# Kernel optimization log

Hardware: AMD Instinct MI355X
Metric: run time of the kernel (lower is better)

## Reference

```python
import jax, jax.numpy as jnp
import numpy as np

D_MODEL = 1024
NHEAD = 16
HEAD_DIM = D_MODEL // NHEAD
LN_EPS = 1e-5


def _layer_norm(x, g, b):
    mu = jnp.mean(x, axis=-1, keepdims=True)
    var = jnp.var(x, axis=-1, keepdims=True)
    return (x - mu) * jax.lax.rsqrt(var + LN_EPS) * g + b


def setup_inputs() -> dict:
    key = jax.random.key(0)
    ks = jax.random.split(key, 12)
    B, S = 2, 2048
    init = 0.02
    return {
        "query": jax.random.normal(ks[0], (B, S, D_MODEL), jnp.float32),
        "key_": jax.random.normal(ks[1], (B, S, D_MODEL), jnp.float32),
        "value": jax.random.normal(ks[2], (B, S, D_MODEL), jnp.float32),
        "Wq": jax.random.normal(ks[3], (D_MODEL, D_MODEL), jnp.float32) * init,
        "bq": jnp.zeros((D_MODEL,), jnp.float32),
        "Wk": jax.random.normal(ks[4], (D_MODEL, D_MODEL), jnp.float32) * init,
        "bk": jnp.zeros((D_MODEL,), jnp.float32),
        "Wv": jax.random.normal(ks[5], (D_MODEL, D_MODEL), jnp.float32) * init,
        "bv": jnp.zeros((D_MODEL,), jnp.float32),
        "Wo": jax.random.normal(ks[6], (D_MODEL, D_MODEL), jnp.float32) * init,
        "bo": jnp.zeros((D_MODEL,), jnp.float32),
        "ln_g": jnp.ones((D_MODEL,), jnp.float32),
        "ln_b": jnp.zeros((D_MODEL,), jnp.float32),
    }


def reference(query, key_, value, Wq, bq, Wk, bk, Wv, bv, Wo, bo, ln_g, ln_b):
    B, T, D = query.shape
    S = key_.shape[1]
    # shared LayerNorm applied to q, k, v inputs (as in the torch module)
    qn = _layer_norm(query, ln_g, ln_b)
    kn = _layer_norm(key_, ln_g, ln_b)
    vn = _layer_norm(value, ln_g, ln_b)
    # projections (torch Linear: x @ W.T + b)
    q = qn @ Wq.T + bq
    k = kn @ Wk.T + bk
    v = vn @ Wv.T + bv
    # [B, H, S, Dh]
    q = q.reshape(B, T, NHEAD, HEAD_DIM).transpose(0, 2, 1, 3)
    k = k.reshape(B, S, NHEAD, HEAD_DIM).transpose(0, 2, 1, 3)
    v = v.reshape(B, S, NHEAD, HEAD_DIM).transpose(0, 2, 1, 3)
    q = q * (HEAD_DIM ** -0.5)
    # [B, H, T, S] score matrix (explicitly materialized, as in source)
    scores = jnp.einsum("bhtd,bhsd->bhts", q, k)
    causal = jnp.triu(jnp.ones((T, S), dtype=bool), k=1)
    scores = jnp.where(causal, -jnp.inf, scores)
    attn = jax.nn.softmax(scores.astype(jnp.float32), axis=-1).astype(query.dtype)
    out = jnp.einsum("bhts,bhsd->bhtd", attn, v)
    out = out.transpose(0, 2, 1, 3).reshape(B, T, D)
    out = out @ Wo.T + bo
    return out, attn
```

## Files before the change

### kernel.cpp

```cpp
#include <hip/hip_runtime.h>
#include <hip/hip_bf16.h>

typedef unsigned short u16;
typedef unsigned int u32;
typedef __bf16 bf16x8 __attribute__((ext_vector_type(8)));
typedef float f32x4 __attribute__((ext_vector_type(4)));

__device__ __forceinline__ u16 f2bf(float f) {
  __hip_bfloat16 h = __float2bfloat16(f);
  u16 u;
  __builtin_memcpy(&u, &h, 2);
  return u;
}

__device__ __forceinline__ void gload16(const u16* g, u16* l) {
  __builtin_amdgcn_global_load_lds(
      (const __attribute__((address_space(1))) u32*)g,
      (__attribute__((address_space(3))) u32*)l, 16, 0, 0);
}

__global__ __launch_bounds__(256) void ln_cast(
    const float* __restrict__ q, const float* __restrict__ k,
    const float* __restrict__ v, const float* __restrict__ g,
    const float* __restrict__ bb, u16* __restrict__ xn) {
  int row = blockIdx.x;
  int tsel = row >> 12;
  int r_in = row & 4095;
  const float* src = (tsel == 0) ? q : (tsel == 1) ? k : v;
  int tid = threadIdx.x;
  float4 x = ((const float4*)(src + (size_t)r_in * 1024))[tid];
  float s  = x.x + x.y + x.z + x.w;
  float ss = x.x * x.x + x.y * x.y + x.z * x.z + x.w * x.w;
  #pragma unroll
  for (int m = 1; m < 64; m <<= 1) { s += __shfl_xor(s, m); ss += __shfl_xor(ss, m); }
  __shared__ float red[8];
  int wid = tid >> 6;
  if ((tid & 63) == 0) { red[wid] = s; red[wid + 4] = ss; }
  __syncthreads();
  s  = red[0] + red[1] + red[2] + red[3];
  ss = red[4] + red[5] + red[6] + red[7];
  float mu  = s * (1.f / 1024.f);
  float var = ss * (1.f / 1024.f) - mu * mu;
  float rs  = rsqrtf(var + 1e-5f);
  float4 gv = ((const float4*)g)[tid];
  float4 bv = ((const float4*)bb)[tid];
  ushort4 o;
  o.x = f2bf((x.x - mu) * rs * gv.x + bv.x);
  o.y = f2bf((x.y - mu) * rs * gv.y + bv.y);
  o.z = f2bf((x.z - mu) * rs * gv.z + bv.z);
  o.w = f2bf((x.w - mu) * rs * gv.w + bv.w);
  ((ushort4*)(xn + (size_t)row * 1024))[tid] = o;
}

__global__ __launch_bounds__(256) void wcast(
    const float* __restrict__ wq, const float* __restrict__ wk,
    const float* __restrict__ wv, const float* __restrict__ wo,
    u16* __restrict__ dst) {
  int i = blockIdx.x * 256 + threadIdx.x;
  int e = i * 4;
  int sel = e >> 20;
  int loc = e & 1048575;
  const float* w = (sel == 0) ? wq : (sel == 1) ? wk : (sel == 2) ? wv : wo;
  float4 x = *(const float4*)(w + loc);
  ushort4 o;
  o.x = f2bf(x.x); o.y = f2bf(x.y); o.z = f2bf(x.z); o.w = f2bf(x.w);
  *(ushort4*)(dst + e) = o;
}

__global__ __launch_bounds__(256) void gemm_nt(
    const u16* __restrict__ A0, const u16* __restrict__ W0,
    const float* __restrict__ bias0, const float* __restrict__ bias1,
    const float* __restrict__ bias2,
    float* __restrict__ oF, u16* __restrict__ oP, u16* __restrict__ oVT,
    int mode) {
  __shared__ alignas(16) u16 Al[128][64];
  __shared__ alignas(16) u16 Bl[128][64];
  int z = blockIdx.z;
  const u16* A = A0 + (size_t)z * 4194304;
  const u16* W = W0 + (size_t)z * 1048576;
  const float* bias = (z == 0) ? bias0 : (z == 1) ? bias1 : bias2;
  int m0 = blockIdx.y * 128, n0 = blockIdx.x * 128;
  int tid = threadIdx.x;
  int lane = tid & 63, wid = tid >> 6;
  int wr = wid >> 1, wc = wid & 1;
  int l15 = lane & 15, lg = lane >> 4;
  int lr = lane >> 3, lc = lane & 7;

  f32x4 acc[4][4];
  #pragma unroll
  for (int i = 0; i < 4; ++i)
    #pragma unroll
    for (int j = 0; j < 4; ++j) acc[i][j] = (f32x4){0.f, 0.f, 0.f, 0.f};

  for (int kt = 0; kt < 1024; kt += 64) {
    __syncthreads();
    #pragma unroll
    for (int qq = 0; qq < 4; ++qq) {
      int rb = (qq * 4 + wid) * 8;
      gload16(A + (size_t)(m0 + rb + lr) * 1024 + kt + lc * 8, &Al[rb][0]);
      gload16(W + (size_t)(n0 + rb + lr) * 1024 + kt + lc * 8, &Bl[rb][0]);
    }
    __syncthreads();
    #pragma unroll
    for (int kb = 0; kb < 2; ++kb) {
      bf16x8 af[4], bw[4];
      #pragma unroll
      for (int i = 0; i < 4; ++i)
        af[i] = *(const bf16x8*)&Al[wr * 64 + i * 16 + l15][kb * 32 + lg * 8];
      #pragma unroll
      for (int j = 0; j < 4; ++j)
        bw[j] = *(const bf16x8*)&Bl[wc * 64 + j * 16 + l15][kb * 32 + lg * 8];
      #pragma unroll
      for (int i = 0; i < 4; ++i)
        #pragma unroll
        for (int j = 0; j < 4; ++j)
          acc[i][j] = __builtin_amdgcn_mfma_f32_16x16x32_bf16(af[i], bw[j], acc[i][j], 0, 0, 0);
    }
  }

  float scale = (mode == 1 && z == 0) ? 0.125f : 1.f;
  #pragma unroll
  for (int i = 0; i < 4; ++i) {
    #pragma unroll
    for (int j = 0; j < 4; ++j) {
      int n = n0 + wc * 64 + j * 16 + l15;
      float bn = bias[n];
      #pragma unroll
      for (int r = 0; r < 4; ++r) {
        int m = m0 + wr * 64 + i * 16 + lg * 4 + r;
        float val = (acc[i][j][r] + bn) * scale;
        if (mode == 0) {
          oF[(size_t)m * 1024 + n] = val;
        } else {
          int b = m >> 11, sIdx = m & 2047, h = n >> 6, d = n & 63;
          if (z == 2) {
            oVT[((size_t)((b * 16 + h) * 64 + d)) * 2048 + sIdx] = f2bf(val);
          } else {
            oP[(size_t)z * 4194304 +
               ((size_t)((b * 16 + h) * 2048 + sIdx)) * 64 + d] = f2bf(val);
          }
        }
      }
    }
  }
}

__global__ __launch_bounds__(256) void attn_kernel(
    const u16* __restrict__ proj, const u16* __restrict__ vt,
    float* __restrict__ attnOut, u16* __restrict__ oat,
    float* __restrict__ linvG) {
  __shared__ alignas(16) u16 Kl[64][64];
  __shared__ alignas(16) u16 Vt[64][64];
  __shared__ alignas(16) u16 Pl[4][16][72];
  const int t0 = blockIdx.x * 64;
  const int bh = blockIdx.y;
  const int tid = threadIdx.x;
  const int lane = tid & 63, w = tid >> 6;
  const int l15 = lane & 15, lg = lane >> 4;
  const int lr = lane >> 3, lc = lane & 7;
  const u16* Q = proj;
  const u16* K = proj + 4194304;
  const u16* VT = vt + (size_t)bh * 131072;

  float* attnB = attnOut + ((size_t)bh * 2048) * 2048;

  {
    const int zc0 = t0 + 64;
    const int rowLen = (2048 - zc0) >> 2;
    const float4 z4 = make_float4(0.f, 0.f, 0.f, 0.f);
    for (int r = w; r < 64; r += 4) {
      float4* rp = (float4*)(attnB + (size_t)(t0 + r) * 2048 + zc0);
      for (int cc = lane; cc < rowLen; cc += 64) rp[cc] = z4;
    }
  }

  bf16x8 qa[2];
  {
    size_t qoff = ((size_t)bh * 2048 + t0 + w * 16 + l15) * 64 + lg * 8;
    qa[0] = *(const bf16x8*)(Q + qoff);
    qa[1] = *(const bf16x8*)(Q + qoff + 32);
  }
  const int jmax = t0 >> 6;
  const int trow_qk = t0 + w * 16 + l15;

  float lsum = 0.f;
  f32x4 acc_o[4];
  #pragma unroll
  for (int c2 = 0; c2 < 4; ++c2) acc_o[c2] = (f32x4){0.f, 0.f, 0.f, 0.f};

  for (int j = 0; j <= jmax; ++j) {
    __syncthreads();
    #pragma unroll
    for (int qq = 0; qq < 2; ++qq) {
      int rb = (qq * 4 + w) * 8;
      gload16(K + ((size_t)bh * 2048 + j * 64 + rb + lr) * 64 + lc * 8, &Kl[rb][0]);
      gload16(VT + (size_t)(rb + lr) * 2048 + j * 64 + lc * 8, &Vt[rb][0]);
    }
    __syncthreads();
    #pragma unroll
    for (int c = 0; c < 4; ++c) {
      f32x4 s = {0.f, 0.f, 0.f, 0.f};
      #pragma unroll
      for (int kb = 0; kb < 2; ++kb) {
        bf16x8 ka = *(const bf16x8*)&Kl[c * 16 + l15][kb * 32 + lg * 8];
        s = __builtin_amdgcn_mfma_f32_16x16x32_bf16(ka, qa[kb], s, 0, 0, 0);
      }
      int col0 = j * 64 + c * 16 + lg * 4;
      float p[4];
      #pragma unroll
      for (int r = 0; r < 4; ++r) {
        float e = __expf(s[r]);
        p[r] = (col0 + r <= trow_qk) ? e : 0.f;
        lsum += p[r];
      }
      *(float4*)&attnB[(size_t)trow_qk * 2048 + col0] =
          make_float4(p[0], p[1], p[2], p[3]);
      ushort4 pk;
      pk.x = f2bf(p[0]); pk.y = f2bf(p[1]); pk.z = f2bf(p[2]); pk.w = f2bf(p[3]);
      *(ushort4*)&Pl[w][l15][c * 16 + lg * 4] = pk;
    }
    __syncthreads();
    #pragma unroll
    for (int kb = 0; kb < 2; ++kb) {
      bf16x8 pa = *(const bf16x8*)&Pl[w][l15][kb * 32 + lg * 8];
      #pragma unroll
      for (int c2 = 0; c2 < 4; ++c2) {
        bf16x8 bv = *(const bf16x8*)&Vt[c2 * 16 + l15][kb * 32 + lg * 8];
        acc_o[c2] = __builtin_amdgcn_mfma_f32_16x16x32_bf16(pa, bv, acc_o[c2], 0, 0, 0);
      }
    }
  }

  lsum += __shfl_xor(lsum, 16);
  lsum += __shfl_xor(lsum, 32);
  float linv = 1.f / lsum;
  if (lg == 0) linvG[(size_t)bh * 2048 + trow_qk] = linv;

  float linv_r[4];
  #pragma unroll
  for (int r = 0; r < 4; ++r) linv_r[r] = __shfl(linv, lg * 4 + r);

  int b = bh >> 4, h = bh & 15;
  #pragma unroll
  for (int c2 = 0; c2 < 4; ++c2) {
    #pragma unroll
    for (int r = 0; r < 4; ++r) {
      int trow = t0 + w * 16 + lg * 4 + r;
      oat[((size_t)(b * 2048 + trow)) * 1024 + h * 64 + c2 * 16 + l15] =
          f2bf(acc_o[c2][r] * linv_r[r]);
    }
  }
}

__global__ __launch_bounds__(256) void rescale_kernel(
    float* __restrict__ attnOut, const float* __restrict__ linvG) {
  const int t0 = blockIdx.x * 64;
  const int bh = blockIdx.y;
  const int tid = threadIdx.x;
  const int lane = tid & 63, w = tid >> 6;
  const int ncol4 = (t0 + 64) >> 2;
  float* attnB = attnOut + ((size_t)bh * 2048) * 2048;
  for (int r = w; r < 64; r += 4) {
    float li = linvG[(size_t)bh * 2048 + t0 + r];
    float4* rp = (float4*)(attnB + (size_t)(t0 + r) * 2048);
    for (int cc = lane; cc < ncol4; cc += 64) {
      float4 x = rp[cc];
      x.x *= li; x.y *= li; x.z *= li; x.w *= li;
      rp[cc] = x;
    }
  }
}

extern "C" void kernel_launch(void* const* d_in, const int* in_sizes, int n_in,
                              void* d_out, int out_size, void* d_ws, size_t ws_size,
                              hipStream_t stream) {
  const float* q    = (const float*)d_in[0];
  const float* k    = (const float*)d_in[1];
  const float* v    = (const float*)d_in[2];
  const float* Wq   = (const float*)d_in[3];
  const float* bq   = (const float*)d_in[4];
  const float* Wk   = (const float*)d_in[5];
  const float* bk   = (const float*)d_in[6];
  const float* Wv   = (const float*)d_in[7];
  const float* bv   = (const float*)d_in[8];
  const float* Wo   = (const float*)d_in[9];
  const float* bo   = (const float*)d_in[10];
  const float* ln_g = (const float*)d_in[11];
  const float* ln_b = (const float*)d_in[12];

  u16* ws   = (u16*)d_ws;
  u16* xn   = ws;
  u16* wb   = ws + 12582912;
  u16* proj = ws + 16777216;
  u16* vt   = ws + 25165824;
  u16* oat  = ws + 29360128;
  float* linvG = (float*)(ws + 33554432);
  float* out  = (float*)d_out;
  float* attn = out + 4194304;

  ln_cast<<<dim3(12288), dim3(256), 0, stream>>>(q, k, v, ln_g, ln_b, xn);
  wcast<<<dim3(4096), dim3(256), 0, stream>>>(Wq, Wk, Wv, Wo, wb);
  gemm_nt<<<dim3(8, 32, 3), dim3(256), 0, stream>>>(xn, wb, bq, bk, bv,
                                                    nullptr, proj, vt, 1);
  attn_kernel<<<dim3(32, 32), dim3(256), 0, stream>>>(proj, vt, attn, oat, linvG);
  rescale_kernel<<<dim3(32, 32), dim3(256), 0, stream>>>(attn, linvG);
  gemm_nt<<<dim3(8, 32, 1), dim3(256), 0, stream>>>(oat, wb + 3 * 1048576, bo,
                                                    bo, bo, out, nullptr, nullptr, 0);
}
```

Baseline: 918.1 us.

## Fuse attention-prob normalization into attention kernel via full-row LDS buffer

The attention kernel now keeps each block's unnormalized bf16 probability rows (32 query rows by 2048 keys) in shared memory. Once row sums are known, it writes the normalized fp32 attention matrix, zero tail included, in a single pass. This removes the separate rescale kernel and its read-modify-write of the large attention output. Blocks shrink to 32 query rows with 512 threads, and each wave handles one 16-column slice, with XOR swizzling of the LDS layouts. The risks are that the stored probabilities are now bf16-rounded before normalization, and that the roughly 128KB of LDS per block limits occupancy.

```diff
diff --git a/kernel.cpp b/kernel.cpp
--- a/kernel.cpp
+++ b/kernel.cpp
@@ -11,6 +11,12 @@
   u16 u;
   __builtin_memcpy(&u, &h, 2);
   return u;
+}
+__device__ __forceinline__ float bf2f(u16 u) {
+  u32 b = ((u32)u) << 16;
+  float f;
+  __builtin_memcpy(&f, &b, 4);
+  return f;
 }
 
 __device__ __forceinline__ void gload16(const u16* g, u16* l) {
@@ -145,128 +151,118 @@
   }
 }
 
-__global__ __launch_bounds__(256) void attn_kernel(
+__global__ __launch_bounds__(512) void attn_kernel(
     const u16* __restrict__ proj, const u16* __restrict__ vt,
-    float* __restrict__ attnOut, u16* __restrict__ oat,
-    float* __restrict__ linvG) {
+    float* __restrict__ attnOut, u16* __restrict__ oat) {
+  __shared__ alignas(16) u16 Ps[32][2048];
   __shared__ alignas(16) u16 Kl[64][64];
   __shared__ alignas(16) u16 Vt[64][64];
-  __shared__ alignas(16) u16 Pl[4][16][72];
-  const int t0 = blockIdx.x * 64;
-  const int bh = blockIdx.y;
+  __shared__ float lred[2][16][4];
+  __shared__ float linv_s[32];
+
+  const int bh = blockIdx.x;
+  const int tb = blockIdx.y;
+  const int t0 = tb * 32;
   const int tid = threadIdx.x;
-  const int lane = tid & 63, w = tid >> 6;
+  const int w = tid >> 6;
+  const int qt = w >> 2;
+  const int c  = w & 3;
+  const int lane = tid & 63;
   const int l15 = lane & 15, lg = lane >> 4;
   const int lr = lane >> 3, lc = lane & 7;
+  const int swz_src = ((lc ^ lr) * 8);
+
   const u16* Q = proj;
   const u16* K = proj + 4194304;
-  const u16* VT = vt + (size_t)bh * 131072;
-
-  float* attnB = attnOut + ((size_t)bh * 2048) * 2048;
-
-  {
-    const int zc0 = t0 + 64;
-    const int rowLen = (2048 - zc0) >> 2;
-    const float4 z4 = make_float4(0.f, 0.f, 0.f, 0.f);
-    for (int r = w; r < 64; r += 4) {
-      float4* rp = (float4*)(attnB + (size_t)(t0 + r) * 2048 + zc0);
-      for (int cc = lane; cc < rowLen; cc += 64) rp[cc] = z4;
-    }
-  }
+  const u16* VTg = vt + (size_t)bh * 131072;
 
   bf16x8 qa[2];
   {
-    size_t qoff = ((size_t)bh * 2048 + t0 + w * 16 + l15) * 64 + lg * 8;
+    size_t qoff = ((size_t)bh * 2048 + t0 + qt * 16 + l15) * 64 + lg * 8;
     qa[0] = *(const bf16x8*)(Q + qoff);
     qa[1] = *(const bf16x8*)(Q + qoff + 32);
   }
-  const int jmax = t0 >> 6;
-  const int trow_qk = t0 + w * 16 + l15;
+  const int jmax = tb >> 1;
+  const int tq = qt * 16 + l15;
+  const int tg = t0 + tq;
+  const int swz_q = (l15 & 7) * 8;
 
   float lsum = 0.f;
-  f32x4 acc_o[4];
-  #pragma unroll
-  for (int c2 = 0; c2 < 4; ++c2) acc_o[c2] = (f32x4){0.f, 0.f, 0.f, 0.f};
+  f32x4 acc_o = {0.f, 0.f, 0.f, 0.f};
 
   for (int j = 0; j <= jmax; ++j) {
     __syncthreads();
-    #pragma unroll
-    for (int qq = 0; qq < 2; ++qq) {
-      int rb = (qq * 4 + w) * 8;
-      gload16(K + ((size_t)bh * 2048 + j * 64 + rb + lr) * 64 + lc * 8, &Kl[rb][0]);
-      gload16(VT + (size_t)(rb + lr) * 2048 + j * 64 + lc * 8, &Vt[rb][0]);
-    }
-    __syncthreads();
-    #pragma unroll
-    for (int c = 0; c < 4; ++c) {
-      f32x4 s = {0.f, 0.f, 0.f, 0.f};
-      #pragma unroll
-      for (int kb = 0; kb < 2; ++kb) {
-        bf16x8 ka = *(const bf16x8*)&Kl[c * 16 + l15][kb * 32 + lg * 8];
-        s = __builtin_amdgcn_mfma_f32_16x16x32_bf16(ka, qa[kb], s, 0, 0, 0);
-      }
-      int col0 = j * 64 + c * 16 + lg * 4;
-      float p[4];
-      #pragma unroll
-      for (int r = 0; r < 4; ++r) {
-        float e = __expf(s[r]);
-        p[r] = (col0 + r <= trow_qk) ? e : 0.f;
-        lsum += p[r];
-      }
-      *(float4*)&attnB[(size_t)trow_qk * 2048 + col0] =
-          make_float4(p[0], p[1], p[2], p[3]);
-      ushort4 pk;
-      pk.x = f2bf(p[0]); pk.y = f2bf(p[1]); pk.z = f2bf(p[2]); pk.w = f2bf(p[3]);
-      *(ushort4*)&Pl[w][l15][c * 16 + lg * 4] = pk;
-    }
+    gload16(K + ((size_t)bh * 2048 + j * 64 + w * 8 + lr) * 64 + swz_src,
+            &Kl[w * 8][0]);
+    gload16(VTg + (size_t)(w * 8 + lr) * 2048 + j * 64 + swz_src,
+            &Vt[w * 8][0]);
+    __syncthreads();
+    f32x4 s4 = {0.f, 0.f, 0.f, 0.f};
+    {
+      bf16x8 ka0 = *(const bf16x8*)&Kl[c * 16 + l15][(lg * 8) ^ swz_q];
+      bf16x8 ka1 = *(const bf16x8*)&Kl[c * 16 + l15][(32 + lg * 8) ^ swz_q];
+      s4 = __builtin_amdgcn_mfma_f32_16x16x32_bf16(ka0, qa[0], s4, 0, 0, 0);
+      s4 = __builtin_amdgcn_mfma_f32_16x16x32_bf16(ka1, qa[1], s4, 0, 0, 0);
+    }
+    int col0 = j * 64 + c * 16 + lg * 4;
+    float p0, p1, p2, p3;
+    p0 = (col0 + 0 <= tg) ? __expf(s4[0]) : 0.f;
+    p1 = (col0 + 1 <= tg) ? __expf(s4[1]) : 0.f;
+    p2 = (col0 + 2 <= tg) ? __expf(s4[2]) : 0.f;
+    p3 = (col0 + 3 <= tg) ? __expf(s4[3]) : 0.f;
+    lsum += (p0 + p1) + (p2 + p3);
+    ushort4 pk;
+    pk.x = f2bf(p0); pk.y = f2bf(p1); pk.z = f2bf(p2); pk.w = f2bf(p3);
+    *(ushort4*)&Ps[tq][col0 ^ swz_q] = pk;
     __syncthreads();
     #pragma unroll
     for (int kb = 0; kb < 2; ++kb) {
-      bf16x8 pa = *(const bf16x8*)&Pl[w][l15][kb * 32 + lg * 8];
-      #pragma unroll
-      for (int c2 = 0; c2 < 4; ++c2) {
-        bf16x8 bv = *(const bf16x8*)&Vt[c2 * 16 + l15][kb * 32 + lg * 8];
-        acc_o[c2] = __builtin_amdgcn_mfma_f32_16x16x32_bf16(pa, bv, acc_o[c2], 0, 0, 0);
-      }
+      bf16x8 pa = *(const bf16x8*)&Ps[tq][(j * 64 + kb * 32 + lg * 8) ^ swz_q];
+      bf16x8 vb = *(const bf16x8*)&Vt[c * 16 + l15][(kb * 32 + lg * 8) ^ swz_q];
+      acc_o = __builtin_amdgcn_mfma_f32_16x16x32_bf16(pa, vb, acc_o, 0, 0, 0);
     }
   }
 
   lsum += __shfl_xor(lsum, 16);
   lsum += __shfl_xor(lsum, 32);
-  float linv = 1.f / lsum;
-  if (lg == 0) linvG[(size_t)bh * 2048 + trow_qk] = linv;
-
-  float linv_r[4];
-  #pragma unroll
-  for (int r = 0; r < 4; ++r) linv_r[r] = __shfl(linv, lg * 4 + r);
-
-  int b = bh >> 4, h = bh & 15;
-  #pragma unroll
-  for (int c2 = 0; c2 < 4; ++c2) {
+  if (lane < 16) lred[qt][l15][c] = lsum;
+  __syncthreads();
+  if (tid < 32) {
+    float t = (lred[tid >> 4][tid & 15][0] + lred[tid >> 4][tid & 15][1]) +
+              (lred[tid >> 4][tid & 15][2] + lred[tid >> 4][tid & 15][3]);
+    linv_s[tid] = 1.f / t;
+  }
+  __syncthreads();
+
+  {
+    int b = bh >> 4, h = bh & 15;
     #pragma unroll
     for (int r = 0; r < 4; ++r) {
-      int trow = t0 + w * 16 + lg * 4 + r;
-      oat[((size_t)(b * 2048 + trow)) * 1024 + h * 64 + c2 * 16 + l15] =
-          f2bf(acc_o[c2][r] * linv_r[r]);
-    }
-  }
-}
-
-__global__ __launch_bounds__(256) void rescale_kernel(
-    float* __restrict__ attnOut, const float* __restrict__ linvG) {
-  const int t0 = blockIdx.x * 64;
-  const int bh = blockIdx.y;
-  const int tid = threadIdx.x;
-  const int lane = tid & 63, w = tid >> 6;
-  const int ncol4 = (t0 + 64) >> 2;
-  float* attnB = attnOut + ((size_t)bh * 2048) * 2048;
-  for (int r = w; r < 64; r += 4) {
-    float li = linvG[(size_t)bh * 2048 + t0 + r];
-    float4* rp = (float4*)(attnB + (size_t)(t0 + r) * 2048);
-    for (int cc = lane; cc < ncol4; cc += 64) {
-      float4 x = rp[cc];
-      x.x *= li; x.y *= li; x.z *= li; x.w *= li;
-      rp[cc] = x;
+      int tl = qt * 16 + lg * 4 + r;
+      oat[((size_t)(b * 2048 + t0 + tl)) * 1024 + h * 64 + c * 16 + l15] =
+          f2bf(acc_o[r] * linv_s[tl]);
+    }
+  }
+
+  {
+    float* attnB = attnOut + (size_t)bh * 2048 * 2048 + (size_t)t0 * 2048;
+    const int zc0 = (jmax + 1) * 64;
+    int row = tid >> 4;
+    int ct  = tid & 15;
+    float li = linv_s[row];
+    int sw = (row & 7) * 8;
+    float4* rp = (float4*)(attnB + (size_t)row * 2048);
+    for (int cc = ct; cc < 512; cc += 16) {
+      int colb = cc * 4;
+      float4 o4;
+      if (colb < zc0) {
+        ushort4 p4 = *(const ushort4*)&Ps[row][colb ^ sw];
+        o4.x = bf2f(p4.x) * li; o4.y = bf2f(p4.y) * li;
+        o4.z = bf2f(p4.z) * li; o4.w = bf2f(p4.w) * li;
+      } else {
+        o4 = make_float4(0.f, 0.f, 0.f, 0.f);
+      }
+      rp[cc] = o4;
     }
   }
 }
@@ -294,7 +290,6 @@
   u16* proj = ws + 16777216;
   u16* vt   = ws + 25165824;
   u16* oat  = ws + 29360128;
-  float* linvG = (float*)(ws + 33554432);
   float* out  = (float*)d_out;
   float* attn = out + 4194304;
 
@@ -302,8 +297,7 @@
   wcast<<<dim3(4096), dim3(256), 0, stream>>>(Wq, Wk, Wv, Wo, wb);
   gemm_nt<<<dim3(8, 32, 3), dim3(256), 0, stream>>>(xn, wb, bq, bk, bv,
                                                     nullptr, proj, vt, 1);
-  attn_kernel<<<dim3(32, 32), dim3(256), 0, stream>>>(proj, vt, attn, oat, linvG);
-  rescale_kernel<<<dim3(32, 32), dim3(256), 0, stream>>>(attn, linvG);
+  attn_kernel<<<dim3(32, 64), dim3(512), 0, stream>>>(proj, vt, attn, oat);
   gemm_nt<<<dim3(8, 32, 1), dim3(256), 0, stream>>>(oat, wb + 3 * 1048576, bo,
                                                     bo, bo, out, nullptr, nullptr, 0);
 }
```

Result: faster. 773.8 us (-15.7%).
